# Performance work log

Measured on AMD Instinct MI355X. Metric: run time of the kernel, lower is better.

Reference implementation:

```python
import jax, jax.numpy as jnp
import numpy as np
from jax import lax

B, L, H = 16, 96, 128  # batch, encoder_input_size (seq/channels), hidden_size


def _same_pad(k):
    # torch Conv2d padding='same' (stride=1, dilation=1): left = (k-1)//2, extra on right
    t = k - 1
    return (t // 2, t - t // 2)


def setup_inputs() -> dict:
    key = jax.random.key(0)
    ks = jax.random.split(key, 10)
    return {
        "hidden": jax.random.normal(ks[0], (B, H), jnp.float32),
        "encoder_outputs": jax.random.normal(ks[1], (B, L, H), jnp.float32),
        "coverage": jax.random.uniform(ks[2], (B, L), jnp.float32),
        # attnConv: Conv2d(L, L, (H, H)) weight [out,in,kh,kw]
        "attn_conv_w": jax.random.normal(ks[3], (L, L, H, H), jnp.float32) * 0.02,
        "attn_conv_b": jax.random.normal(ks[4], (L,), jnp.float32) * 0.02,
        # cvgConv: Conv2d(L, L, (1, H))
        "cvg_conv_w": jax.random.normal(ks[5], (L, L, 1, H), jnp.float32) * 0.02,
        "cvg_conv_b": jax.random.normal(ks[6], (L,), jnp.float32) * 0.02,
        # decoderAttnLinear: Linear(H, H)
        "dec_w": jax.random.normal(ks[7], (H, H), jnp.float32) * 0.02,
        "dec_b": jax.random.normal(ks[8], (H,), jnp.float32) * 0.02,
        # v: Parameter [batch, hidden]
        "v": jax.random.normal(ks[9], (B, H), jnp.float32) * 0.1,
    }


def reference(hidden, encoder_outputs, coverage, attn_conv_w, attn_conv_b,
              cvg_conv_w, cvg_conv_b, dec_w, dec_b, v):
    dn = ("NCHW", "OIHW", "NCHW")
    # encoder features: conv over [B, L, 1, H] with (H, H) kernel, 'same' padding -> [B, L, 1, H]
    x = encoder_outputs[:, :, None, :]
    enc_f = lax.conv_general_dilated(
        x, attn_conv_w, (1, 1), [_same_pad(H), _same_pad(H)], dimension_numbers=dn
    ) + attn_conv_b[None, :, None, None]
    # decoder features: Linear(hidden) -> [B, 1, 1, H]
    dec_f = (hidden @ dec_w.T + dec_b)[:, None, None, :]
    # coverage features: conv over [B, L, 1, 1] with (1, H) kernel, 'same' -> [B, L, 1, 1]
    c = coverage[:, :, None, None]
    cvg_f = lax.conv_general_dilated(
        c, cvg_conv_w, (1, 1), [(0, 0), _same_pad(H)], dimension_numbers=dn
    ) + cvg_conv_b[None, :, None, None]
    # additive attention: tanh of summed features, project with v, softmax over L
    feats = jnp.tanh((enc_f + dec_f + cvg_f).reshape(B, L, H))
    scores = jnp.einsum("blh,bh->bl", feats, v)
    attn = jax.nn.softmax(scores, axis=1)
    new_coverage = coverage + attn
    context = jnp.einsum("bl,blh->bh", attn, encoder_outputs)
    return context, attn, new_coverage
```

## Files before the change

### kernel.cpp

```cpp
#include <hip/hip_runtime.h>
#include <hip/hip_bf16.h>
#include <math.h>

#define BB 16
#define LL 96
#define HH 128

typedef __attribute__((ext_vector_type(8))) short short8;
typedef __attribute__((ext_vector_type(4))) float f32x4;

#define WS_W    0
#define WS_E    589824
#define WS_DEC  983040
#define WS_CVG  985088
#define WS_SC   986624
#define WS_P    988160

__global__ __launch_bounds__(256) void prep_kernel(
        const float* __restrict__ hidden,
        const float* __restrict__ enc,
        const float* __restrict__ coverage,
        const float* __restrict__ attn_w,
        const float* __restrict__ cvg_w,
        const float* __restrict__ cvg_b,
        const float* __restrict__ dec_w,
        const float* __restrict__ dec_b,
        float* __restrict__ ws) {
    const int bid = blockIdx.x;
    const int tid = threadIdx.x;
    if (bid < 96) {
        const int i = bid;
        unsigned short* wout = (unsigned short*)(ws + WS_W);
        for (int idx = tid; idx < LL * HH; idx += 256) {
            const int o = idx >> 7, e = idx & 127;
            const int esrc = e ^ ((o & 7) << 3);
            float v = attn_w[(((size_t)o * LL + i) * HH + 63) * HH + esrc];
            __hip_bfloat16 h = __float2bfloat16(v);
            wout[(size_t)i * LL * HH + idx] = *(unsigned short*)&h;
        }
    } else if (bid < 112) {
        const int b = bid - 96;
        float* eout = ws + WS_E + (size_t)b * LL * 256;
        for (int idx = tid; idx < LL * 256; idx += 256) {
            const int i = idx >> 8, t = idx & 255;
            eout[idx] = (t >= 63 && t < 191) ? enc[((size_t)b * LL + i) * HH + (t - 63)] : 0.f;
        }
    } else {
        const int b = bid - 112;
        __shared__ float hid[HH];
        __shared__ float cov[LL];
        if (tid < HH) hid[tid] = hidden[b * HH + tid];
        if (tid < LL) cov[tid] = coverage[b * LL + tid];
        __syncthreads();
        if (tid < HH) {
            float acc = dec_b[tid];
            for (int k = 0; k < HH; ++k) acc += hid[k] * dec_w[tid * HH + k];
            ws[WS_DEC + b * HH + tid] = acc;
        } else if (tid < HH + LL) {
            const int t = tid - HH;
            float a2 = cvg_b[t];
            for (int i2 = 0; i2 < LL; ++i2)
                a2 += cov[i2] * cvg_w[((size_t)t * LL + i2) * HH + 63];
            ws[WS_CVG + b * LL + t] = a2;
        }
    }
}

__global__ __launch_bounds__(256) void mfma_kernel(float* __restrict__ ws) {
    const int kc = blockIdx.x;
    const int b  = blockIdx.y;
    const int tid  = threadIdx.x;
    const int lane = tid & 63;
    const int wg   = tid >> 6;
    const int lo   = lane & 15;
    const int hi   = lane >> 4;

    __shared__ __align__(16) short Abuf[LL * HH];
    __shared__ __align__(16) float Ebuf[256];

    f32x4 acc[6][2];
#pragma unroll
    for (int a = 0; a < 6; ++a)
#pragma unroll
        for (int c = 0; c < 2; ++c) acc[a][c] = f32x4{0.f, 0.f, 0.f, 0.f};

    const short* wsrc = (const short*)(ws + WS_W);
    const float* esrc = ws + WS_E + (size_t)b * LL * 256;

    for (int ii = 0; ii < 3; ++ii) {
        const int ig = kc * 3 + ii;
        __syncthreads();
        {
            const short8* s8 = (const short8*)(wsrc + (size_t)ig * LL * HH);
            short8* d8 = (short8*)Abuf;
#pragma unroll
            for (int t = 0; t < 6; ++t) d8[tid + t * 256] = s8[tid + t * 256];
            if (tid < 64)
                ((float4*)Ebuf)[tid] = ((const float4*)(esrc + ig * 256))[tid];
        }
        __syncthreads();

#pragma unroll
        for (int s = 0; s < 4; ++s) {
            short8 af[6];
#pragma unroll
            for (int ot = 0; ot < 6; ++ot) {
                const int o = ot * 16 + lo;
                const int idx8 = o * 16 + (((s << 2) + hi) ^ (o & 7));
                af[ot] = ((const short8*)Abuf)[idx8];
            }
#pragma unroll
            for (int wt = 0; wt < 2; ++wt) {
                const int t0 = s * 32 + hi * 8 + wg * 32 + wt * 16 + lo;
                union { short8 s8; __hip_bfloat16 h[8]; } bf;
#pragma unroll
                for (int j = 0; j < 8; ++j) bf.h[j] = __float2bfloat16(Ebuf[t0 + j]);
#pragma unroll
                for (int ot = 0; ot < 6; ++ot)
                    acc[ot][wt] = __builtin_amdgcn_mfma_f32_16x16x32_bf16(
                        af[ot], bf.s8, acc[ot][wt], 0, 0, 0);
            }
        }
    }

    float* dst = ws + WS_P + ((size_t)kc * BB + b) * LL * HH;
#pragma unroll
    for (int ot = 0; ot < 6; ++ot)
#pragma unroll
        for (int wt = 0; wt < 2; ++wt)
#pragma unroll
            for (int r = 0; r < 4; ++r) {
                const int o = ot * 16 + hi * 4 + r;
                const int w = wg * 32 + wt * 16 + lo;
                dst[o * HH + w] = acc[ot][wt][r];
            }
}

__global__ __launch_bounds__(128) void reduce_kernel(
        const float* __restrict__ attn_b,
        const float* __restrict__ vvec,
        float* __restrict__ ws) {
    const int o = blockIdx.x;
    const int b = blockIdx.y;
    const int h = threadIdx.x;
    const float* p = ws + WS_P + (size_t)b * LL * HH + o * HH + h;
    float sum = 0.f;
#pragma unroll
    for (int kc = 0; kc < 32; ++kc) sum += p[(size_t)kc * BB * LL * HH];
    float ef = sum + attn_b[o] + ws[WS_DEC + b * HH + h] + ws[WS_CVG + b * LL + o];
    float s = tanhf(ef) * vvec[b * HH + h];
#pragma unroll
    for (int off = 32; off > 0; off >>= 1) s += __shfl_down(s, off, 64);
    __shared__ float r2[2];
    if ((h & 63) == 0) r2[h >> 6] = s;
    __syncthreads();
    if (h == 0) ws[WS_SC + b * LL + o] = r2[0] + r2[1];
}

__global__ void finalize_kernel(const float* __restrict__ ws_scores,
                                const float* __restrict__ coverage,
                                const float* __restrict__ enc,
                                float* __restrict__ out) {
    int b = blockIdx.x;
    int t = threadIdx.x;
    __shared__ float sc[LL];
    __shared__ float at[LL];
    if (t < LL) sc[t] = ws_scores[b * LL + t];
    __syncthreads();

    float mx = -1e30f;
    for (int l = 0; l < LL; ++l) mx = fmaxf(mx, sc[l]);
    float sum = 0.f;
    for (int l = 0; l < LL; ++l) sum += expf(sc[l] - mx);

    if (t < LL) {
        float a = expf(sc[t] - mx) / sum;
        at[t] = a;
        out[BB * HH + b * LL + t] = a;
        out[BB * HH + BB * LL + b * LL + t] = coverage[b * LL + t] + a;
    }
    __syncthreads();

    float ctx = 0.f;
    for (int l = 0; l < LL; ++l) ctx += at[l] * enc[(b * LL + l) * HH + t];
    out[b * HH + t] = ctx;
}

extern "C" void kernel_launch(void* const* d_in, const int* in_sizes, int n_in,
                              void* d_out, int out_size, void* d_ws, size_t ws_size,
                              hipStream_t stream) {
    const float* hidden   = (const float*)d_in[0];
    const float* enc      = (const float*)d_in[1];
    const float* coverage = (const float*)d_in[2];
    const float* attn_w   = (const float*)d_in[3];
    const float* attn_b   = (const float*)d_in[4];
    const float* cvg_w    = (const float*)d_in[5];
    const float* cvg_b    = (const float*)d_in[6];
    const float* dec_w    = (const float*)d_in[7];
    const float* dec_b    = (const float*)d_in[8];
    const float* vvec     = (const float*)d_in[9];
    float* out = (float*)d_out;
    float* ws = (float*)d_ws;

    prep_kernel<<<128, 256, 0, stream>>>(hidden, enc, coverage, attn_w,
                                         cvg_w, cvg_b, dec_w, dec_b, ws);
    mfma_kernel<<<dim3(32, BB), 256, 0, stream>>>(ws);
    reduce_kernel<<<dim3(LL, BB), 128, 0, stream>>>(attn_b, vvec, ws);
    finalize_kernel<<<BB, HH, 0, stream>>>(ws + WS_SC, coverage, enc, out);
}
```

Measured before the change: 49.08 us.

## Double-buffer MFMA staging, pre-convert encoder to bf16, half partials, fuse finalize

```diff
diff --git a/kernel.cpp b/kernel.cpp
--- a/kernel.cpp
+++ b/kernel.cpp
@@ -1,5 +1,6 @@
 #include <hip/hip_runtime.h>
 #include <hip/hip_bf16.h>
+#include <hip/hip_fp16.h>
 #include <math.h>
 
 #define BB 16
@@ -9,12 +10,13 @@
 typedef __attribute__((ext_vector_type(8))) short short8;
 typedef __attribute__((ext_vector_type(4))) float f32x4;
 
-#define WS_W    0
-#define WS_E    589824
-#define WS_DEC  983040
-#define WS_CVG  985088
-#define WS_SC   986624
-#define WS_P    988160
+#define WS_W_OFF   0
+#define WS_E_OFF   2359296
+#define WS_DEC_OFF 4030464
+#define WS_CVG_OFF 4038656
+#define WS_SC_OFF  4044800
+#define WS_CNT_OFF 4050944
+#define WS_P_OFF   4051008
 
 __global__ __launch_bounds__(256) void prep_kernel(
         const float* __restrict__ hidden,
@@ -25,12 +27,12 @@
         const float* __restrict__ cvg_b,
         const float* __restrict__ dec_w,
         const float* __restrict__ dec_b,
-        float* __restrict__ ws) {
+        char* __restrict__ wsb) {
     const int bid = blockIdx.x;
     const int tid = threadIdx.x;
     if (bid < 96) {
         const int i = bid;
-        unsigned short* wout = (unsigned short*)(ws + WS_W);
+        unsigned short* wout = (unsigned short*)(wsb + WS_W_OFF);
         for (int idx = tid; idx < LL * HH; idx += 256) {
             const int o = idx >> 7, e = idx & 127;
             const int esrc = e ^ ((o & 7) << 3);
@@ -40,33 +42,51 @@
         }
     } else if (bid < 112) {
         const int b = bid - 96;
-        float* eout = ws + WS_E + (size_t)b * LL * 256;
-        for (int idx = tid; idx < LL * 256; idx += 256) {
-            const int i = idx >> 8, t = idx & 255;
-            eout[idx] = (t >= 63 && t < 191) ? enc[((size_t)b * LL + i) * HH + (t - 63)] : 0.f;
+        unsigned int* eout = (unsigned int*)(wsb + WS_E_OFF) + (size_t)b * LL * 272;
+        const float* esrc = enc + (size_t)b * LL * HH;
+        for (int idx = tid; idx < LL * 272; idx += 256) {
+            const int i = idx / 272, c = idx % 272;
+            int t0 = -1, t1 = -1;
+            if (c < 128) { t0 = 2 * c; t1 = 2 * c + 1; }
+            else if (c >= 129 && c < 257) { int q = c - 129; t0 = 2 * q + 1; t1 = 2 * q + 2; }
+            unsigned int lo16 = 0, hi16 = 0;
+            if (t0 >= 63 && t0 < 191) {
+                __hip_bfloat16 h = __float2bfloat16(esrc[i * HH + t0 - 63]);
+                lo16 = *(unsigned short*)&h;
+            }
+            if (t1 >= 63 && t1 < 191) {
+                __hip_bfloat16 h = __float2bfloat16(esrc[i * HH + t1 - 63]);
+                hi16 = *(unsigned short*)&h;
+            }
+            eout[idx] = lo16 | (hi16 << 16);
         }
     } else {
         const int b = bid - 112;
+        float* decf = (float*)(wsb + WS_DEC_OFF);
+        float* cvgf = (float*)(wsb + WS_CVG_OFF);
         __shared__ float hid[HH];
         __shared__ float cov[LL];
         if (tid < HH) hid[tid] = hidden[b * HH + tid];
         if (tid < LL) cov[tid] = coverage[b * LL + tid];
+        if (tid == 255)
+            __hip_atomic_store((int*)(wsb + WS_CNT_OFF) + b, 0,
+                               __ATOMIC_RELAXED, __HIP_MEMORY_SCOPE_AGENT);
         __syncthreads();
         if (tid < HH) {
             float acc = dec_b[tid];
             for (int k = 0; k < HH; ++k) acc += hid[k] * dec_w[tid * HH + k];
-            ws[WS_DEC + b * HH + tid] = acc;
+            decf[b * HH + tid] = acc;
         } else if (tid < HH + LL) {
             const int t = tid - HH;
             float a2 = cvg_b[t];
             for (int i2 = 0; i2 < LL; ++i2)
                 a2 += cov[i2] * cvg_w[((size_t)t * LL + i2) * HH + 63];
-            ws[WS_CVG + b * LL + t] = a2;
+            cvgf[b * LL + t] = a2;
         }
     }
 }
 
-__global__ __launch_bounds__(256) void mfma_kernel(float* __restrict__ ws) {
+__global__ __launch_bounds__(256) void mfma_kernel(char* __restrict__ wsb) {
     const int kc = blockIdx.x;
     const int b  = blockIdx.y;
     const int tid  = threadIdx.x;
@@ -75,115 +95,145 @@
     const int lo   = lane & 15;
     const int hi   = lane >> 4;
 
-    __shared__ __align__(16) short Abuf[LL * HH];
-    __shared__ __align__(16) float Ebuf[256];
+    __shared__ __align__(16) short Abuf[2][LL * HH];
+    __shared__ __align__(16) unsigned int Ebuf[2][272];
+
+    const char* wbase = wsb + WS_W_OFF;
+    const unsigned int* esrc = (const unsigned int*)(wsb + WS_E_OFF)
+                               + ((size_t)b * LL + kc * 3) * 272;
+    __half* Pp = (__half*)(wsb + WS_P_OFF);
 
     f32x4 acc[6][2];
 #pragma unroll
-    for (int a = 0; a < 6; ++a)
-#pragma unroll
-        for (int c = 0; c < 2; ++c) acc[a][c] = f32x4{0.f, 0.f, 0.f, 0.f};
-
-    const short* wsrc = (const short*)(ws + WS_W);
-    const float* esrc = ws + WS_E + (size_t)b * LL * 256;
-
-    for (int ii = 0; ii < 3; ++ii) {
-        const int ig = kc * 3 + ii;
-        __syncthreads();
-        {
-            const short8* s8 = (const short8*)(wsrc + (size_t)ig * LL * HH);
-            short8* d8 = (short8*)Abuf;
-#pragma unroll
-            for (int t = 0; t < 6; ++t) d8[tid + t * 256] = s8[tid + t * 256];
-            if (tid < 64)
-                ((float4*)Ebuf)[tid] = ((const float4*)(esrc + ig * 256))[tid];
-        }
-        __syncthreads();
-
+    for (int ot = 0; ot < 6; ++ot)
+#pragma unroll
+        for (int wt = 0; wt < 2; ++wt) acc[ot][wt] = f32x4{0.f, 0.f, 0.f, 0.f};
+
+    auto stageA = [&](int r, int buf) {
+        const char* gA = wbase + (size_t)(kc * 3 + r) * (LL * HH * 2);
+        char* lA = (char*)&Abuf[buf][0];
+#pragma unroll
+        for (int c = 0; c < 6; ++c) {
+            __builtin_amdgcn_global_load_lds(
+                (const __attribute__((address_space(1))) void*)(gA + c * 4096 + tid * 16),
+                (__attribute__((address_space(3))) void*)(lA + c * 4096 + wg * 1024),
+                16, 0, 0);
+        }
+    };
+    auto stageE = [&](int r, int buf) {
+        if (tid < 68) {
+            uint4 v = *(const uint4*)(esrc + r * 272 + tid * 4);
+            *(uint4*)&Ebuf[buf][tid * 4] = v;
+        }
+    };
+    auto compute = [&](int buf) {
+        const short8* A8 = (const short8*)&Abuf[buf][0];
+        const unsigned int* row = &Ebuf[buf][0];
 #pragma unroll
         for (int s = 0; s < 4; ++s) {
             short8 af[6];
 #pragma unroll
             for (int ot = 0; ot < 6; ++ot) {
                 const int o = ot * 16 + lo;
-                const int idx8 = o * 16 + (((s << 2) + hi) ^ (o & 7));
-                af[ot] = ((const short8*)Abuf)[idx8];
+                af[ot] = A8[o * 16 + (((s << 2) + hi) ^ (lo & 7))];
             }
 #pragma unroll
             for (int wt = 0; wt < 2; ++wt) {
                 const int t0 = s * 32 + hi * 8 + wg * 32 + wt * 16 + lo;
-                union { short8 s8; __hip_bfloat16 h[8]; } bf;
-#pragma unroll
-                for (int j = 0; j < 8; ++j) bf.h[j] = __float2bfloat16(Ebuf[t0 + j]);
+                const unsigned int* arr = row + ((lo & 1) ? 129 : 0) + (t0 >> 1);
+                union { uint4 u; short8 s8; } bf;
+                bf.u.x = arr[0]; bf.u.y = arr[1]; bf.u.z = arr[2]; bf.u.w = arr[3];
 #pragma unroll
                 for (int ot = 0; ot < 6; ++ot)
                     acc[ot][wt] = __builtin_amdgcn_mfma_f32_16x16x32_bf16(
                         af[ot], bf.s8, acc[ot][wt], 0, 0, 0);
             }
         }
-    }
-
-    float* dst = ws + WS_P + ((size_t)kc * BB + b) * LL * HH;
+    };
+
+    stageA(0, 0); stageE(0, 0);
+    __syncthreads();
+    stageA(1, 1); stageE(1, 1);
+    compute(0);
+    __syncthreads();
+    stageA(2, 0); stageE(2, 0);
+    compute(1);
+    __syncthreads();
+    compute(0);
+
 #pragma unroll
     for (int ot = 0; ot < 6; ++ot)
 #pragma unroll
-        for (int wt = 0; wt < 2; ++wt)
+        for (int wt = 0; wt < 2; ++wt) {
+            const int w = wg * 32 + wt * 16 + lo;
 #pragma unroll
             for (int r = 0; r < 4; ++r) {
                 const int o = ot * 16 + hi * 4 + r;
-                const int w = wg * 32 + wt * 16 + lo;
-                dst[o * HH + w] = acc[ot][wt][r];
-            }
-}
-
-__global__ __launch_bounds__(128) void reduce_kernel(
+                Pp[((size_t)(kc * BB + b) * LL + o) * HH + w] =
+                    __float2half(acc[ot][wt][r]);
+            }
+        }
+}
+
+__global__ __launch_bounds__(128) void reduceF_kernel(
         const float* __restrict__ attn_b,
         const float* __restrict__ vvec,
-        float* __restrict__ ws) {
+        const float* __restrict__ coverage,
+        const float* __restrict__ enc,
+        char* __restrict__ wsb,
+        float* __restrict__ out) {
     const int o = blockIdx.x;
     const int b = blockIdx.y;
     const int h = threadIdx.x;
-    const float* p = ws + WS_P + (size_t)b * LL * HH + o * HH + h;
+    const __half* p = (const __half*)(wsb + WS_P_OFF) + ((size_t)b * LL + o) * HH + h;
+    const float* dec = (const float*)(wsb + WS_DEC_OFF);
+    const float* cvg = (const float*)(wsb + WS_CVG_OFF);
+    float* sc_ws = (float*)(wsb + WS_SC_OFF);
+    int* cnt = (int*)(wsb + WS_CNT_OFF);
+
     float sum = 0.f;
 #pragma unroll
-    for (int kc = 0; kc < 32; ++kc) sum += p[(size_t)kc * BB * LL * HH];
-    float ef = sum + attn_b[o] + ws[WS_DEC + b * HH + h] + ws[WS_CVG + b * LL + o];
+    for (int kc = 0; kc < 32; ++kc)
+        sum += __half2float(p[(size_t)kc * BB * LL * HH]);
+    float ef = sum + attn_b[o] + dec[b * HH + h] + cvg[b * LL + o];
     float s = tanhf(ef) * vvec[b * HH + h];
 #pragma unroll
     for (int off = 32; off > 0; off >>= 1) s += __shfl_down(s, off, 64);
+
     __shared__ float r2[2];
+    __shared__ int isLast;
     if ((h & 63) == 0) r2[h >> 6] = s;
     __syncthreads();
-    if (h == 0) ws[WS_SC + b * LL + o] = r2[0] + r2[1];
-}
-
-__global__ void finalize_kernel(const float* __restrict__ ws_scores,
-                                const float* __restrict__ coverage,
-                                const float* __restrict__ enc,
-                                float* __restrict__ out) {
-    int b = blockIdx.x;
-    int t = threadIdx.x;
-    __shared__ float sc[LL];
-    __shared__ float at[LL];
-    if (t < LL) sc[t] = ws_scores[b * LL + t];
-    __syncthreads();
-
+    if (h == 0) {
+        float sc = r2[0] + r2[1];
+        __hip_atomic_store(&sc_ws[b * LL + o], sc,
+                           __ATOMIC_RELEASE, __HIP_MEMORY_SCOPE_AGENT);
+        int old = __hip_atomic_fetch_add(&cnt[b], 1,
+                                         __ATOMIC_ACQ_REL, __HIP_MEMORY_SCOPE_AGENT);
+        isLast = (old == LL - 1);
+    }
+    __syncthreads();
+    if (!isLast) return;
+
+    __shared__ float scl[LL], atl[LL];
+    if (h < LL)
+        scl[h] = __hip_atomic_load(&sc_ws[b * LL + h],
+                                   __ATOMIC_ACQUIRE, __HIP_MEMORY_SCOPE_AGENT);
+    __syncthreads();
     float mx = -1e30f;
-    for (int l = 0; l < LL; ++l) mx = fmaxf(mx, sc[l]);
-    float sum = 0.f;
-    for (int l = 0; l < LL; ++l) sum += expf(sc[l] - mx);
-
-    if (t < LL) {
-        float a = expf(sc[t] - mx) / sum;
-        at[t] = a;
-        out[BB * HH + b * LL + t] = a;
-        out[BB * HH + BB * LL + b * LL + t] = coverage[b * LL + t] + a;
+    for (int l = 0; l < LL; ++l) mx = fmaxf(mx, scl[l]);
+    float den = 0.f;
+    for (int l = 0; l < LL; ++l) den += expf(scl[l] - mx);
+    if (h < LL) {
+        float a = expf(scl[h] - mx) / den;
+        atl[h] = a;
+        out[BB * HH + b * LL + h] = a;
+        out[BB * HH + BB * LL + b * LL + h] = coverage[b * LL + h] + a;
     }
     __syncthreads();
-
-    float ctx = 0.f;
-    for (int l = 0; l < LL; ++l) ctx += at[l] * enc[(b * LL + l) * HH + t];
-    out[b * HH + t] = ctx;
+    float c = 0.f;
+    for (int l = 0; l < LL; ++l) c += atl[l] * enc[((size_t)b * LL + l) * HH + h];
+    out[b * HH + h] = c;
 }
 
 extern "C" void kernel_launch(void* const* d_in, const int* in_sizes, int n_in,
@@ -200,11 +250,11 @@
     const float* dec_b    = (const float*)d_in[8];
     const float* vvec     = (const float*)d_in[9];
     float* out = (float*)d_out;
-    float* ws = (float*)d_ws;
+    char* wsb = (char*)d_ws;
 
     prep_kernel<<<128, 256, 0, stream>>>(hidden, enc, coverage, attn_w,
-                                         cvg_w, cvg_b, dec_w, dec_b, ws);
-    mfma_kernel<<<dim3(32, BB), 256, 0, stream>>>(ws);
-    reduce_kernel<<<dim3(LL, BB), 128, 0, stream>>>(attn_b, vvec, ws);
-    finalize_kernel<<<BB, HH, 0, stream>>>(ws + WS_SC, coverage, enc, out);
-}
+                                         cvg_w, cvg_b, dec_w, dec_b, wsb);
+    mfma_kernel<<<dim3(32, BB), 256, 0, stream>>>(wsb);
+    reduceF_kernel<<<dim3(LL, BB), 128, 0, stream>>>(attn_b, vvec, coverage,
+                                                     enc, wsb, out);
+}
```

After: 112.1 us. 128% more time.

## Pre-pack weights and encoder into MFMA fragment layouts and drop LDS staging

Applied to the files above, without the earlier changes.

```diff
diff --git a/kernel.cpp b/kernel.cpp
--- a/kernel.cpp
+++ b/kernel.cpp
@@ -9,12 +9,12 @@
 typedef __attribute__((ext_vector_type(8))) short short8;
 typedef __attribute__((ext_vector_type(4))) float f32x4;
 
-#define WS_W    0
-#define WS_E    589824
-#define WS_DEC  983040
-#define WS_CVG  985088
-#define WS_SC   986624
-#define WS_P    988160
+#define WS_W_OFF   0
+#define WS_E_OFF   2359296
+#define WS_DEC_OFF 4030464
+#define WS_CVG_OFF 4038656
+#define WS_SC_OFF  4044800
+#define WS_P_OFF   4050944
 
 __global__ __launch_bounds__(256) void prep_kernel(
         const float* __restrict__ hidden,
@@ -25,28 +25,44 @@
         const float* __restrict__ cvg_b,
         const float* __restrict__ dec_w,
         const float* __restrict__ dec_b,
-        float* __restrict__ ws) {
+        char* __restrict__ wsb) {
     const int bid = blockIdx.x;
     const int tid = threadIdx.x;
     if (bid < 96) {
         const int i = bid;
-        unsigned short* wout = (unsigned short*)(ws + WS_W);
+        unsigned short* wout = (unsigned short*)(wsb + WS_W_OFF);
         for (int idx = tid; idx < LL * HH; idx += 256) {
-            const int o = idx >> 7, e = idx & 127;
-            const int esrc = e ^ ((o & 7) << 3);
-            float v = attn_w[(((size_t)o * LL + i) * HH + 63) * HH + esrc];
+            const int o = idx >> 7, m = idx & 127;
+            float v = attn_w[(((size_t)o * LL + i) * HH + 63) * HH + m];
             __hip_bfloat16 h = __float2bfloat16(v);
-            wout[(size_t)i * LL * HH + idx] = *(unsigned short*)&h;
+            const int f = (i * 4 + (m >> 5)) * 6 + (o >> 4);
+            const int off = (((m >> 3) & 3) * 16 + (o & 15)) * 8 + (m & 7);
+            wout[(size_t)f * 512 + off] = *(unsigned short*)&h;
         }
     } else if (bid < 112) {
         const int b = bid - 96;
-        float* eout = ws + WS_E + (size_t)b * LL * 256;
-        for (int idx = tid; idx < LL * 256; idx += 256) {
-            const int i = idx >> 8, t = idx & 255;
-            eout[idx] = (t >= 63 && t < 191) ? enc[((size_t)b * LL + i) * HH + (t - 63)] : 0.f;
+        unsigned int* eout = (unsigned int*)(wsb + WS_E_OFF) + (size_t)b * LL * 272;
+        const float* esrc = enc + (size_t)b * LL * HH;
+        for (int idx = tid; idx < LL * 272; idx += 256) {
+            const int i = idx / 272, c = idx % 272;
+            int t0 = -1, t1 = -1;
+            if (c < 128) { t0 = 2 * c; t1 = 2 * c + 1; }
+            else if (c >= 129 && c < 257) { int q = c - 129; t0 = 2 * q + 1; t1 = 2 * q + 2; }
+            unsigned int lo16 = 0, hi16 = 0;
+            if (t0 >= 63 && t0 < 191) {
+                __hip_bfloat16 h = __float2bfloat16(esrc[i * HH + t0 - 63]);
+                lo16 = *(unsigned short*)&h;
+            }
+            if (t1 >= 63 && t1 < 191) {
+                __hip_bfloat16 h = __float2bfloat16(esrc[i * HH + t1 - 63]);
+                hi16 = *(unsigned short*)&h;
+            }
+            eout[idx] = lo16 | (hi16 << 16);
         }
     } else {
         const int b = bid - 112;
+        float* decf = (float*)(wsb + WS_DEC_OFF);
+        float* cvgf = (float*)(wsb + WS_CVG_OFF);
         __shared__ float hid[HH];
         __shared__ float cov[LL];
         if (tid < HH) hid[tid] = hidden[b * HH + tid];
@@ -55,18 +71,18 @@
         if (tid < HH) {
             float acc = dec_b[tid];
             for (int k = 0; k < HH; ++k) acc += hid[k] * dec_w[tid * HH + k];
-            ws[WS_DEC + b * HH + tid] = acc;
+            decf[b * HH + tid] = acc;
         } else if (tid < HH + LL) {
             const int t = tid - HH;
             float a2 = cvg_b[t];
             for (int i2 = 0; i2 < LL; ++i2)
                 a2 += cov[i2] * cvg_w[((size_t)t * LL + i2) * HH + 63];
-            ws[WS_CVG + b * LL + t] = a2;
+            cvgf[b * LL + t] = a2;
         }
     }
 }
 
-__global__ __launch_bounds__(256) void mfma_kernel(float* __restrict__ ws) {
+__global__ __launch_bounds__(256) void mfma_kernel(char* __restrict__ wsb) {
     const int kc = blockIdx.x;
     const int b  = blockIdx.y;
     const int tid  = threadIdx.x;
@@ -74,87 +90,81 @@
     const int wg   = tid >> 6;
     const int lo   = lane & 15;
     const int hi   = lane >> 4;
-
-    __shared__ __align__(16) short Abuf[LL * HH];
-    __shared__ __align__(16) float Ebuf[256];
-
-    f32x4 acc[6][2];
-#pragma unroll
-    for (int a = 0; a < 6; ++a)
-#pragma unroll
-        for (int c = 0; c < 2; ++c) acc[a][c] = f32x4{0.f, 0.f, 0.f, 0.f};
-
-    const short* wsrc = (const short*)(ws + WS_W);
-    const float* esrc = ws + WS_E + (size_t)b * LL * 256;
-
-    for (int ii = 0; ii < 3; ++ii) {
-        const int ig = kc * 3 + ii;
-        __syncthreads();
-        {
-            const short8* s8 = (const short8*)(wsrc + (size_t)ig * LL * HH);
-            short8* d8 = (short8*)Abuf;
-#pragma unroll
-            for (int t = 0; t < 6; ++t) d8[tid + t * 256] = s8[tid + t * 256];
-            if (tid < 64)
-                ((float4*)Ebuf)[tid] = ((const float4*)(esrc + ig * 256))[tid];
-        }
-        __syncthreads();
-
+    const int oh   = wg >> 1;
+    const int wh   = wg & 1;
+
+    const unsigned short* Wf = (const unsigned short*)(wsb + WS_W_OFF);
+    const unsigned int*   Eb = (const unsigned int*)(wsb + WS_E_OFF)
+                               + ((size_t)b * LL + kc * 3) * 272;
+    float* Pp = (float*)(wsb + WS_P_OFF);
+
+    f32x4 acc[3][4];
+#pragma unroll
+    for (int t = 0; t < 3; ++t)
+#pragma unroll
+        for (int wt = 0; wt < 4; ++wt) acc[t][wt] = f32x4{0.f, 0.f, 0.f, 0.f};
+
+#pragma unroll
+    for (int r = 0; r < 3; ++r) {
+        const unsigned int* erow = Eb + r * 272 + ((lo & 1) ? 129 : 0);
+        const unsigned short* frow = Wf + (size_t)((kc * 3 + r) * 4) * 6 * 512 + lane * 8;
 #pragma unroll
         for (int s = 0; s < 4; ++s) {
-            short8 af[6];
-#pragma unroll
-            for (int ot = 0; ot < 6; ++ot) {
-                const int o = ot * 16 + lo;
-                const int idx8 = o * 16 + (((s << 2) + hi) ^ (o & 7));
-                af[ot] = ((const short8*)Abuf)[idx8];
-            }
-#pragma unroll
-            for (int wt = 0; wt < 2; ++wt) {
-                const int t0 = s * 32 + hi * 8 + wg * 32 + wt * 16 + lo;
-                union { short8 s8; __hip_bfloat16 h[8]; } bf;
-#pragma unroll
-                for (int j = 0; j < 8; ++j) bf.h[j] = __float2bfloat16(Ebuf[t0 + j]);
-#pragma unroll
-                for (int ot = 0; ot < 6; ++ot)
-                    acc[ot][wt] = __builtin_amdgcn_mfma_f32_16x16x32_bf16(
-                        af[ot], bf.s8, acc[ot][wt], 0, 0, 0);
+            short8 af[3];
+#pragma unroll
+            for (int t = 0; t < 3; ++t)
+                af[t] = *(const short8*)(frow + (s * 6 + oh * 3 + t) * 512);
+#pragma unroll
+            for (int wt = 0; wt < 4; ++wt) {
+                const int t0 = s * 32 + wh * 64 + wt * 16 + hi * 8 + lo;
+                const unsigned int* a = erow + (t0 >> 1);
+                union { uint4 u; short8 s8; } bf;
+                bf.u.x = a[0]; bf.u.y = a[1]; bf.u.z = a[2]; bf.u.w = a[3];
+#pragma unroll
+                for (int t = 0; t < 3; ++t)
+                    acc[t][wt] = __builtin_amdgcn_mfma_f32_16x16x32_bf16(
+                        af[t], bf.s8, acc[t][wt], 0, 0, 0);
             }
         }
     }
 
-    float* dst = ws + WS_P + ((size_t)kc * BB + b) * LL * HH;
-#pragma unroll
-    for (int ot = 0; ot < 6; ++ot)
-#pragma unroll
-        for (int wt = 0; wt < 2; ++wt)
-#pragma unroll
-            for (int r = 0; r < 4; ++r) {
-                const int o = ot * 16 + hi * 4 + r;
-                const int w = wg * 32 + wt * 16 + lo;
-                dst[o * HH + w] = acc[ot][wt][r];
-            }
+    float* dst = Pp + (size_t)(kc * BB + b) * LL * HH;
+#pragma unroll
+    for (int t = 0; t < 3; ++t)
+#pragma unroll
+        for (int wt = 0; wt < 4; ++wt) {
+            const int w = wh * 64 + wt * 16 + lo;
+#pragma unroll
+            for (int rr = 0; rr < 4; ++rr) {
+                const int o = (oh * 3 + t) * 16 + hi * 4 + rr;
+                dst[o * HH + w] = acc[t][wt][rr];
+            }
+        }
 }
 
 __global__ __launch_bounds__(128) void reduce_kernel(
         const float* __restrict__ attn_b,
         const float* __restrict__ vvec,
-        float* __restrict__ ws) {
+        char* __restrict__ wsb) {
     const int o = blockIdx.x;
     const int b = blockIdx.y;
     const int h = threadIdx.x;
-    const float* p = ws + WS_P + (size_t)b * LL * HH + o * HH + h;
+    const float* p = (const float*)(wsb + WS_P_OFF) + ((size_t)b * LL + o) * HH + h;
+    const float* dec = (const float*)(wsb + WS_DEC_OFF);
+    const float* cvg = (const float*)(wsb + WS_CVG_OFF);
+    float* sc_ws = (float*)(wsb + WS_SC_OFF);
+
     float sum = 0.f;
 #pragma unroll
     for (int kc = 0; kc < 32; ++kc) sum += p[(size_t)kc * BB * LL * HH];
-    float ef = sum + attn_b[o] + ws[WS_DEC + b * HH + h] + ws[WS_CVG + b * LL + o];
+    float ef = sum + attn_b[o] + dec[b * HH + h] + cvg[b * LL + o];
     float s = tanhf(ef) * vvec[b * HH + h];
 #pragma unroll
     for (int off = 32; off > 0; off >>= 1) s += __shfl_down(s, off, 64);
     __shared__ float r2[2];
     if ((h & 63) == 0) r2[h >> 6] = s;
     __syncthreads();
-    if (h == 0) ws[WS_SC + b * LL + o] = r2[0] + r2[1];
+    if (h == 0) sc_ws[b * LL + o] = r2[0] + r2[1];
 }
 
 __global__ void finalize_kernel(const float* __restrict__ ws_scores,
@@ -182,7 +192,8 @@
     __syncthreads();
 
     float ctx = 0.f;
-    for (int l = 0; l < LL; ++l) ctx += at[l] * enc[(b * LL + l) * HH + t];
+#pragma unroll 8
+    for (int l = 0; l < LL; ++l) ctx += at[l] * enc[((size_t)b * LL + l) * HH + t];
     out[b * HH + t] = ctx;
 }
 
@@ -200,11 +211,12 @@
     const float* dec_b    = (const float*)d_in[8];
     const float* vvec     = (const float*)d_in[9];
     float* out = (float*)d_out;
-    float* ws = (float*)d_ws;
+    char* wsb = (char*)d_ws;
 
     prep_kernel<<<128, 256, 0, stream>>>(hidden, enc, coverage, attn_w,
-                                         cvg_w, cvg_b, dec_w, dec_b, ws);
-    mfma_kernel<<<dim3(32, BB), 256, 0, stream>>>(ws);
-    reduce_kernel<<<dim3(LL, BB), 128, 0, stream>>>(attn_b, vvec, ws);
-    finalize_kernel<<<BB, HH, 0, stream>>>(ws + WS_SC, coverage, enc, out);
-}
+                                         cvg_w, cvg_b, dec_w, dec_b, wsb);
+    mfma_kernel<<<dim3(32, BB), 256, 0, stream>>>(wsb);
+    reduce_kernel<<<dim3(LL, BB), 128, 0, stream>>>(attn_b, vvec, wsb);
+    finalize_kernel<<<BB, HH, 0, stream>>>((const float*)(wsb + WS_SC_OFF),
+                                           coverage, enc, out);
+}
```

Measured after the change: 63.91 us. +30.2%, slower.
